# Optimization experiments

Hardware: AMD Instinct MI355X
Metric: run time of the kernel (lower is better)

Reference implementation:

```python
import jax, jax.numpy as jnp
import numpy as np

N = 4096      # nnode
F = 128       # feature_dim
E = 64        # embed_dim
P_EDGE = 0.01 # edge probability (~41 avg degree)
NEG = -9e15
ALPHA = 0.2   # leaky relu slope


def _xavier(key, shape):
    lim = float(np.sqrt(6.0 / (shape[0] + shape[1])))
    return jax.random.uniform(key, shape, minval=-lim, maxval=lim, dtype=jnp.float32)


def setup_inputs() -> dict:
    key = jax.random.key(0)
    ks = jax.random.split(key, 14)
    features = jax.random.normal(ks[0], (N, F), dtype=jnp.float32)
    eye = jnp.eye(N, dtype=jnp.float32)

    def make_adj(k):
        a = (jax.random.uniform(k, (N, N)) < P_EDGE).astype(jnp.float32)
        return jnp.maximum(a, eye)  # self loop so no empty rows

    return {
        "features": features,
        "geo_adj": make_adj(ks[1]),
        "forward_adj": make_adj(ks[2]),
        "backward_adj": make_adj(ks[3]),
        "weight": _xavier(ks[4], (E, F)),
        "Wf": _xavier(ks[5], (F, E)),
        "af1": jax.random.normal(ks[6], (E,), dtype=jnp.float32) * 0.1,
        "af2": jax.random.normal(ks[7], (E,), dtype=jnp.float32) * 0.1,
        "Wb": _xavier(ks[8], (F, E)),
        "ab1": jax.random.normal(ks[9], (E,), dtype=jnp.float32) * 0.1,
        "ab2": jax.random.normal(ks[10], (E,), dtype=jnp.float32) * 0.1,
        "Wg": _xavier(ks[11], (F, E)),
        "ag1": jax.random.normal(ks[12], (E,), dtype=jnp.float32) * 0.1,
        "ag2": jax.random.normal(ks[13], (E,), dtype=jnp.float32) * 0.1,
    }


def _mean_neighbors(adj, feat):
    # pre_weight: row-normalized neighbor averaging, (N,N) @ (N,F)
    deg = jnp.clip(jnp.sum(adj, axis=1, keepdims=True), 1.0, None)
    return (adj @ feat) / deg


def _attention(feat, mask_feat, adj, W, a1, a2):
    # GAT-style additive attention with masked softmax over neighbors
    h = feat @ W        # (N, E)
    hm = mask_feat @ W  # (N, E)
    e = jax.nn.leaky_relu((h @ a1)[:, None] + (hm @ a2)[None, :], negative_slope=ALPHA)  # (N, N)
    e = jnp.where(adj > 0, e, NEG)
    return jax.nn.softmax(e, axis=1)  # (N, N)


def reference(features, geo_adj, forward_adj, backward_adj, weight,
              Wf, af1, af2, Wb, ab1, ab2, Wg, ag1, ag2):
    t = features  # (N, F)
    mask_f = _mean_neighbors(forward_adj, t)
    mask_b = _mean_neighbors(backward_adj, t)
    mask_g = _mean_neighbors(geo_adj, t)

    w_f = _attention(t, mask_f, forward_adj, Wf, af1, af2)
    w_b = _attention(t, mask_b, backward_adj, Wb, ab1, ab2)
    w_g = _attention(t, mask_g, geo_adj, Wg, ag1, ag2)

    # get_mask_matrix_i/_j broadcast-mul + sum(1) == attn @ t (or attn.T @ t)
    x = weight @ t.T                  # (E, N)
    x_fwd = weight @ (w_f @ t).T      # mask_matrix_i
    x_bwd = weight @ (w_b.T @ t).T    # mask_matrix_j (transposed)
    x_geo = weight @ (w_g @ t).T      # mask_matrix_i

    return jnp.concatenate([x, x_fwd, x_bwd, x_geo], axis=0)  # (4E, N)
```

## Files before the change

### kernel.cpp

```cpp
#include <hip/hip_runtime.h>

#define NN 4096
#define FF 128
#define EE 64

typedef unsigned short u16;
typedef unsigned long long u64;
typedef float vf4 __attribute__((ext_vector_type(4)));

__device__ __forceinline__ float lrelu(float x) { return x > 0.f ? x : 0.2f * x; }

__global__ __launch_bounds__(256)
void k_feat(const float* __restrict__ t, const float* __restrict__ weight,
            const float* __restrict__ Wf, const float* __restrict__ af1, const float* __restrict__ af2,
            const float* __restrict__ Wb, const float* __restrict__ ab1, const float* __restrict__ ab2,
            const float* __restrict__ Wg, const float* __restrict__ ag1, const float* __restrict__ ag2,
            float* __restrict__ u, float* __restrict__ s1, float* __restrict__ p,
            float* __restrict__ out, int* __restrict__ ccnt)
{
    __shared__ float ww[64 * 129];
    __shared__ float tt[16 * 130];
    __shared__ float vv[6 * FF];
    __shared__ float uacc[64 * 17];
    const float* Ws[3]  = {Wf, Wb, Wg};
    const float* a1s[3] = {af1, ab1, ag1};
    const float* a2s[3] = {af2, ab2, ag2};
    int b = blockIdx.x, tid = threadIdx.x;
    int n0 = b * 16;
    if (b < 16) ccnt[b * 256 + tid] = 0;
    const float4* w4 = reinterpret_cast<const float4*>(weight);
    for (int i = tid; i < 2048; i += 256) {
        float4 v = w4[i];
        int fi = i * 4, e = fi >> 7, q = fi & 127;
        float* dst = &ww[e * 129 + q];
        dst[0] = v.x; dst[1] = v.y; dst[2] = v.z; dst[3] = v.w;
    }
    const float4* t4 = reinterpret_cast<const float4*>(t + (size_t)n0 * FF);
    for (int i = tid; i < 512; i += 256) {
        float4 v = t4[i];
        int fi = i * 4, nd = fi >> 7, q = fi & 127;
        float* dst = &tt[nd * 130 + q];
        dst[0] = v.x; dst[1] = v.y; dst[2] = v.z; dst[3] = v.w;
    }
    for (int idx = tid; idx < 6 * FF; idx += 256) {
        int vi = idx >> 7, f = idx & (FF - 1), dd = vi >> 1;
        const float* a = (vi & 1) ? a2s[dd] : a1s[dd];
        const float* W = Ws[dd] + (size_t)f * EE;
        float s = 0.f;
        #pragma unroll 8
        for (int e = 0; e < EE; ++e) s += W[e] * a[e];
        vv[idx] = s;
    }
    __syncthreads();
    int g = tid >> 6, lane = tid & 63;
    for (int k = 0; k < 4; ++k) {
        int nd = g * 4 + k;
        const float* trow = &tt[nd * 130];
        const float* wrow = &ww[lane * 129];
        float acc = 0.f;
        #pragma unroll 16
        for (int q = 0; q < 128; ++q) acc += wrow[q] * trow[q];
        u[(size_t)(n0 + nd) * EE + lane] = acc;
        uacc[lane * 17 + nd] = acc;
        float t0 = trow[lane], t1 = trow[64 + lane];
        for (int vi = 0; vi < 6; ++vi) {
            float x = t0 * vv[vi * FF + lane] + t1 * vv[vi * FF + 64 + lane];
            for (int off = 32; off; off >>= 1) x += __shfl_xor(x, off);
            if (lane == 0) {
                int dd = vi >> 1;
                if (vi & 1) p[dd * NN + n0 + nd] = x; else s1[dd * NN + n0 + nd] = x;
            }
        }
    }
    __syncthreads();
    int e = tid >> 2, io = (tid & 3) * 4;
    float* orow = out + (size_t)e * NN + n0 + io;
    orow[0] = uacc[e * 17 + io];
    orow[1] = uacc[e * 17 + io + 1];
    orow[2] = uacc[e * 17 + io + 2];
    orow[3] = uacc[e * 17 + io + 3];
}

__global__ __launch_bounds__(256, 8)
void k_scan(const float* __restrict__ Af, const float* __restrict__ Ab, const float* __restrict__ Ag,
            const float* __restrict__ p,
            u16* __restrict__ csr, int* __restrict__ cnt, float* __restrict__ s2,
            u16* __restrict__ csc, int* __restrict__ ccnt, int stride)
{
    int wid = threadIdx.x >> 6, lane = threadIdx.x & 63;
    int gr = blockIdx.x * 4 + wid;
    int d = gr >> 12, r = gr & (NN - 1);
    const float* A = d == 0 ? Af : (d == 1 ? Ab : Ag);
    const vf4* row4 = reinterpret_cast<const vf4*>(A + (size_t)r * NN);
    const float* pd = p + d * NN;

    u64 mask = 0ull;
    #pragma unroll
    for (int j = 0; j < 16; ++j) {
        vf4 L = __builtin_nontemporal_load(row4 + j * 64 + lane);
        unsigned mm = (L.x != 0.f ? 1u : 0u) | (L.y != 0.f ? 2u : 0u) |
                      (L.z != 0.f ? 4u : 0u) | (L.w != 0.f ? 8u : 0u);
        mask |= ((u64)mm) << (j * 4);
    }

    int lc = __popcll(mask);
    int sc = lc;
    for (int off = 1; off < 64; off <<= 1) {
        int o = __shfl_up(sc, off);
        if (lane >= off) sc += o;
    }
    int total = __shfl(sc, 63);
    int pos = sc - lc;
    u16* crow = csr + (size_t)gr * stride;
    float q = 0.f;
    u64 m = mask;
    while (m) {
        int b = __ffsll(m) - 1;
        m &= m - 1;
        int col = ((b >> 2) << 8) + (lane << 2) + (b & 3);
        if (pos < stride) crow[pos] = (u16)col;
        pos++;
        q += pd[col];
        if (d == 1) {
            int cp = atomicAdd(&ccnt[col], 1);
            if (cp < stride) csc[(size_t)col * stride + cp] = (u16)r;
        }
    }
    for (int off = 32; off; off >>= 1) q += __shfl_xor(q, off);
    if (lane == 0) {
        cnt[gr] = total;
        s2[gr] = q / fmaxf((float)total, 1.f);
    }
}

__global__ void k_zb(const float* __restrict__ s1, const float* __restrict__ s2,
                     const u16* __restrict__ csr, const int* __restrict__ cnt, int stride,
                     float* __restrict__ Zb)
{
    int tid = threadIdx.x, wave = tid >> 6, lane = tid & 63;
    int j = blockIdx.x * 4 + wave;
    int gr = NN + j;
    int nnz = min(cnt[gr], stride);
    const u16* crow = csr + (size_t)gr * stride;
    float s1j = s1[gr];
    const float* s2b = s2 + NN;
    float z = 0.f;
    if (lane < nnz)      z += __expf(lrelu(s1j + s2b[crow[lane]]));
    if (lane + 64 < nnz) z += __expf(lrelu(s1j + s2b[crow[lane + 64]]));
    for (int off = 32; off; off >>= 1) z += __shfl_xor(z, off);
    if (lane == 0) Zb[j] = z;
}

__global__ __launch_bounds__(256)
void k_out(const float* __restrict__ u,
           const float* __restrict__ s1, const float* __restrict__ s2,
           const float* __restrict__ Zb,
           const u16* __restrict__ csr, const int* __restrict__ cnt,
           const u16* __restrict__ csc, const int* __restrict__ ccnt, int stride,
           float* __restrict__ out)
{
    __shared__ float oacc[16 * 66];
    int gr0 = blockIdx.x * 16;
    int d = gr0 >> 12, i0 = gr0 & (NN - 1);
    int wid = threadIdx.x >> 6, lane = threadIdx.x & 63;
    for (int k = 0; k < 4; ++k) {
        int lr = k * 4 + wid;
        int i = i0 + lr;
        int gr = gr0 + lr;
        int nnz;
        int c0v = 0, c1v = 0;
        float w0v = 0.f, w1v = 0.f;
        if (d == 1) {
            nnz = min(ccnt[i], stride);
            const u16* cc = csc + (size_t)i * stride;
            float s2i = s2[NN + i];
            if (lane < nnz)      { int j = cc[lane];      c0v = j; w0v = __expf(lrelu(s1[NN + j] + s2i)) / Zb[j]; }
            if (lane + 64 < nnz) { int j = cc[lane + 64]; c1v = j; w1v = __expf(lrelu(s1[NN + j] + s2i)) / Zb[j]; }
        } else {
            nnz = min(cnt[gr], stride);
            const u16* crow = csr + (size_t)gr * stride;
            float s1i = s1[gr];
            const float* s2d = s2 + d * NN;
            float z = 0.f;
            if (lane < nnz)      { int c = crow[lane];      c0v = c; w0v = __expf(lrelu(s1i + s2d[c])); z += w0v; }
            if (lane + 64 < nnz) { int c = crow[lane + 64]; c1v = c; w1v = __expf(lrelu(s1i + s2d[c])); z += w1v; }
            for (int off = 32; off; off >>= 1) z += __shfl_xor(z, off);
            float invz = z > 0.f ? 1.f / z : 0.f;
            w0v *= invz; w1v *= invz;
        }
        float a0 = 0.f, a1 = 0.f;
        int n0 = nnz < 64 ? nnz : 64;
        int kk = 0;
        for (; kk + 1 < n0; kk += 2) {
            int ca = __shfl(c0v, kk), cb = __shfl(c0v, kk + 1);
            float wa = __shfl(w0v, kk), wb = __shfl(w0v, kk + 1);
            a0 += wa * u[(size_t)ca * EE + lane];
            a1 += wb * u[(size_t)cb * EE + lane];
        }
        if (kk < n0)
            a0 += __shfl(w0v, kk) * u[(size_t)__shfl(c0v, kk) * EE + lane];
        int n1 = nnz - 64;
        kk = 0;
        for (; kk + 1 < n1; kk += 2) {
            int ca = __shfl(c1v, kk), cb = __shfl(c1v, kk + 1);
            float wa = __shfl(w1v, kk), wb = __shfl(w1v, kk + 1);
            a0 += wa * u[(size_t)ca * EE + lane];
            a1 += wb * u[(size_t)cb * EE + lane];
        }
        if (kk < n1)
            a0 += __shfl(w1v, kk) * u[(size_t)__shfl(c1v, kk) * EE + lane];
        oacc[lr * 66 + lane] = a0 + a1;
    }
    __syncthreads();
    int e = threadIdx.x >> 2, io = (threadIdx.x & 3) * 4;
    int base = 64 + (d << 6);
    float* orow = out + (size_t)(base + e) * NN + i0 + io;
    orow[0] = oacc[(io    ) * 66 + e];
    orow[1] = oacc[(io + 1) * 66 + e];
    orow[2] = oacc[(io + 2) * 66 + e];
    orow[3] = oacc[(io + 3) * 66 + e];
}

extern "C" void kernel_launch(void* const* d_in, const int* in_sizes, int n_in,
                              void* d_out, int out_size, void* d_ws, size_t ws_size,
                              hipStream_t stream)
{
    const float* t   = (const float*)d_in[0];
    const float* Ag  = (const float*)d_in[1];
    const float* Af  = (const float*)d_in[2];
    const float* Ab  = (const float*)d_in[3];
    const float* W   = (const float*)d_in[4];
    const float* Wf  = (const float*)d_in[5];
    const float* af1 = (const float*)d_in[6];
    const float* af2 = (const float*)d_in[7];
    const float* Wb  = (const float*)d_in[8];
    const float* ab1 = (const float*)d_in[9];
    const float* ab2 = (const float*)d_in[10];
    const float* Wg  = (const float*)d_in[11];
    const float* ag1 = (const float*)d_in[12];
    const float* ag2 = (const float*)d_in[13];
    float* out = (float*)d_out;

    float* ws = (float*)d_ws;
    float* s1  = ws;
    float* p   = s1 + 3 * NN;
    float* s2  = p + 3 * NN;
    float* Zb  = s2 + 3 * NN;
    float* u   = Zb + NN;
    int*   cnt  = (int*)(u + (size_t)NN * EE);
    int*   ccnt = cnt + 3 * NN;
    u16*   csr  = (u16*)(ccnt + NN);

    size_t base_bytes = ((char*)csr) - ((char*)d_ws);
    int stride = 128;
    if (base_bytes + (size_t)4 * NN * 128 * 2 > ws_size) stride = 96;
    if (base_bytes + (size_t)4 * NN * 96 * 2 > ws_size)  stride = 64;
    u16* csc = csr + (size_t)3 * NN * stride;

    k_feat<<<NN / 16, 256, 0, stream>>>(t, W, Wf, af1, af2, Wb, ab1, ab2, Wg, ag1, ag2,
                                        u, s1, p, out, ccnt);
    k_scan<<<3 * NN / 4, 256, 0, stream>>>(Af, Ab, Ag, p, csr, cnt, s2, csc, ccnt, stride);
    k_zb<<<NN / 4, 256, 0, stream>>>(s1, s2, csr, cnt, stride, Zb);
    k_out<<<3 * NN / 16, 256, 0, stream>>>(u, s1, s2, Zb, csr, cnt, csc, ccnt, stride, out);
}
```

Measured before the change: 262.2 us.

## Parallelize attention-vector precompute per wave, pack s1/invZ, widen k_out blocks

In k_feat, the per-feature W·a dot products move from a serial 64-iteration loop per thread to one wave per item with a shuffle reduction, with the attention vectors staged in shared memory first. k_zb now writes a packed (s1, 1/Z) pair, so k_out does one float2 load and a multiply instead of two loads and a divide. k_out switches to 1024-thread blocks with one wave per row instead of four rows per wave, which exposes more parallelism, but the output store becomes scalar instead of four per thread.

```diff
diff --git a/kernel.cpp b/kernel.cpp
--- a/kernel.cpp
+++ b/kernel.cpp
@@ -21,13 +21,19 @@
     __shared__ float ww[64 * 129];
     __shared__ float tt[16 * 130];
     __shared__ float vv[6 * FF];
+    __shared__ float aa[6 * 64];
     __shared__ float uacc[64 * 17];
     const float* Ws[3]  = {Wf, Wb, Wg};
     const float* a1s[3] = {af1, ab1, ag1};
     const float* a2s[3] = {af2, ab2, ag2};
-    int b = blockIdx.x, tid = threadIdx.x;
+    int b = blockIdx.x, tid = threadIdx.x, wid = tid >> 6, lane = tid & 63;
     int n0 = b * 16;
     if (b < 16) ccnt[b * 256 + tid] = 0;
+    for (int i = tid; i < 384; i += 256) {
+        int vi = i >> 6, e = i & 63, dd = vi >> 1;
+        const float* a = (vi & 1) ? a2s[dd] : a1s[dd];
+        aa[i] = a[e];
+    }
     const float4* w4 = reinterpret_cast<const float4*>(weight);
     for (int i = tid; i < 2048; i += 256) {
         float4 v = w4[i];
@@ -42,19 +48,16 @@
         float* dst = &tt[nd * 130 + q];
         dst[0] = v.x; dst[1] = v.y; dst[2] = v.z; dst[3] = v.w;
     }
-    for (int idx = tid; idx < 6 * FF; idx += 256) {
-        int vi = idx >> 7, f = idx & (FF - 1), dd = vi >> 1;
-        const float* a = (vi & 1) ? a2s[dd] : a1s[dd];
-        const float* W = Ws[dd] + (size_t)f * EE;
-        float s = 0.f;
-        #pragma unroll 8
-        for (int e = 0; e < EE; ++e) s += W[e] * a[e];
-        vv[idx] = s;
-    }
-    __syncthreads();
-    int g = tid >> 6, lane = tid & 63;
+    __syncthreads();
+    for (int item = wid; item < 768; item += 4) {
+        int vi = item >> 7, f = item & 127, dd = vi >> 1;
+        float prod = Ws[dd][(size_t)f * EE + lane] * aa[vi * 64 + lane];
+        for (int off = 32; off; off >>= 1) prod += __shfl_xor(prod, off);
+        if (lane == 0) vv[vi * FF + f] = prod;
+    }
+    __syncthreads();
     for (int k = 0; k < 4; ++k) {
-        int nd = g * 4 + k;
+        int nd = wid * 4 + k;
         const float* trow = &tt[nd * 130];
         const float* wrow = &ww[lane * 129];
         float acc = 0.f;
@@ -135,7 +138,7 @@
 
 __global__ void k_zb(const float* __restrict__ s1, const float* __restrict__ s2,
                      const u16* __restrict__ csr, const int* __restrict__ cnt, int stride,
-                     float* __restrict__ Zb)
+                     float2* __restrict__ zpack)
 {
     int tid = threadIdx.x, wave = tid >> 6, lane = tid & 63;
     int j = blockIdx.x * 4 + wave;
@@ -148,13 +151,13 @@
     if (lane < nnz)      z += __expf(lrelu(s1j + s2b[crow[lane]]));
     if (lane + 64 < nnz) z += __expf(lrelu(s1j + s2b[crow[lane + 64]]));
     for (int off = 32; off; off >>= 1) z += __shfl_xor(z, off);
-    if (lane == 0) Zb[j] = z;
-}
-
-__global__ __launch_bounds__(256)
+    if (lane == 0) zpack[j] = make_float2(s1j, z > 0.f ? 1.f / z : 0.f);
+}
+
+__global__ __launch_bounds__(1024)
 void k_out(const float* __restrict__ u,
            const float* __restrict__ s1, const float* __restrict__ s2,
-           const float* __restrict__ Zb,
+           const float2* __restrict__ zpack,
            const u16* __restrict__ csr, const int* __restrict__ cnt,
            const u16* __restrict__ csc, const int* __restrict__ ccnt, int stride,
            float* __restrict__ out)
@@ -162,63 +165,57 @@
     __shared__ float oacc[16 * 66];
     int gr0 = blockIdx.x * 16;
     int d = gr0 >> 12, i0 = gr0 & (NN - 1);
-    int wid = threadIdx.x >> 6, lane = threadIdx.x & 63;
-    for (int k = 0; k < 4; ++k) {
-        int lr = k * 4 + wid;
-        int i = i0 + lr;
-        int gr = gr0 + lr;
-        int nnz;
-        int c0v = 0, c1v = 0;
-        float w0v = 0.f, w1v = 0.f;
-        if (d == 1) {
-            nnz = min(ccnt[i], stride);
-            const u16* cc = csc + (size_t)i * stride;
-            float s2i = s2[NN + i];
-            if (lane < nnz)      { int j = cc[lane];      c0v = j; w0v = __expf(lrelu(s1[NN + j] + s2i)) / Zb[j]; }
-            if (lane + 64 < nnz) { int j = cc[lane + 64]; c1v = j; w1v = __expf(lrelu(s1[NN + j] + s2i)) / Zb[j]; }
-        } else {
-            nnz = min(cnt[gr], stride);
-            const u16* crow = csr + (size_t)gr * stride;
-            float s1i = s1[gr];
-            const float* s2d = s2 + d * NN;
-            float z = 0.f;
-            if (lane < nnz)      { int c = crow[lane];      c0v = c; w0v = __expf(lrelu(s1i + s2d[c])); z += w0v; }
-            if (lane + 64 < nnz) { int c = crow[lane + 64]; c1v = c; w1v = __expf(lrelu(s1i + s2d[c])); z += w1v; }
-            for (int off = 32; off; off >>= 1) z += __shfl_xor(z, off);
-            float invz = z > 0.f ? 1.f / z : 0.f;
-            w0v *= invz; w1v *= invz;
-        }
-        float a0 = 0.f, a1 = 0.f;
-        int n0 = nnz < 64 ? nnz : 64;
-        int kk = 0;
-        for (; kk + 1 < n0; kk += 2) {
-            int ca = __shfl(c0v, kk), cb = __shfl(c0v, kk + 1);
-            float wa = __shfl(w0v, kk), wb = __shfl(w0v, kk + 1);
-            a0 += wa * u[(size_t)ca * EE + lane];
-            a1 += wb * u[(size_t)cb * EE + lane];
-        }
-        if (kk < n0)
-            a0 += __shfl(w0v, kk) * u[(size_t)__shfl(c0v, kk) * EE + lane];
-        int n1 = nnz - 64;
-        kk = 0;
-        for (; kk + 1 < n1; kk += 2) {
-            int ca = __shfl(c1v, kk), cb = __shfl(c1v, kk + 1);
-            float wa = __shfl(w1v, kk), wb = __shfl(w1v, kk + 1);
-            a0 += wa * u[(size_t)ca * EE + lane];
-            a1 += wb * u[(size_t)cb * EE + lane];
-        }
-        if (kk < n1)
-            a0 += __shfl(w1v, kk) * u[(size_t)__shfl(c1v, kk) * EE + lane];
-        oacc[lr * 66 + lane] = a0 + a1;
-    }
-    __syncthreads();
-    int e = threadIdx.x >> 2, io = (threadIdx.x & 3) * 4;
+    int tid = threadIdx.x, wid = tid >> 6, lane = tid & 63;
+    int lr = wid;
+    int i = i0 + lr;
+    int gr = gr0 + lr;
+    int nnz;
+    int c0v = 0, c1v = 0;
+    float w0v = 0.f, w1v = 0.f;
+    if (d == 1) {
+        nnz = min(ccnt[i], stride);
+        const u16* cc = csc + (size_t)i * stride;
+        float s2i = s2[NN + i];
+        if (lane < nnz)      { int j = cc[lane];      float2 z = zpack[j]; c0v = j; w0v = __expf(lrelu(z.x + s2i)) * z.y; }
+        if (lane + 64 < nnz) { int j = cc[lane + 64]; float2 z = zpack[j]; c1v = j; w1v = __expf(lrelu(z.x + s2i)) * z.y; }
+    } else {
+        nnz = min(cnt[gr], stride);
+        const u16* crow = csr + (size_t)gr * stride;
+        float s1i = s1[gr];
+        const float* s2d = s2 + d * NN;
+        float z = 0.f;
+        if (lane < nnz)      { int c = crow[lane];      c0v = c; w0v = __expf(lrelu(s1i + s2d[c])); z += w0v; }
+        if (lane + 64 < nnz) { int c = crow[lane + 64]; c1v = c; w1v = __expf(lrelu(s1i + s2d[c])); z += w1v; }
+        for (int off = 32; off; off >>= 1) z += __shfl_xor(z, off);
+        float invz = z > 0.f ? 1.f / z : 0.f;
+        w0v *= invz; w1v *= invz;
+    }
+    float a0 = 0.f, a1 = 0.f;
+    int n0 = nnz < 64 ? nnz : 64;
+    int kk = 0;
+    for (; kk + 1 < n0; kk += 2) {
+        int ca = __shfl(c0v, kk), cb = __shfl(c0v, kk + 1);
+        float wa = __shfl(w0v, kk), wb = __shfl(w0v, kk + 1);
+        a0 += wa * u[(size_t)ca * EE + lane];
+        a1 += wb * u[(size_t)cb * EE + lane];
+    }
+    if (kk < n0)
+        a0 += __shfl(w0v, kk) * u[(size_t)__shfl(c0v, kk) * EE + lane];
+    int n1 = nnz - 64;
+    kk = 0;
+    for (; kk + 1 < n1; kk += 2) {
+        int ca = __shfl(c1v, kk), cb = __shfl(c1v, kk + 1);
+        float wa = __shfl(w1v, kk), wb = __shfl(w1v, kk + 1);
+        a0 += wa * u[(size_t)ca * EE + lane];
+        a1 += wb * u[(size_t)cb * EE + lane];
+    }
+    if (kk < n1)
+        a0 += __shfl(w1v, kk) * u[(size_t)__shfl(c1v, kk) * EE + lane];
+    oacc[lr * 66 + lane] = a0 + a1;
+    __syncthreads();
+    int e = tid >> 4, io = tid & 15;
     int base = 64 + (d << 6);
-    float* orow = out + (size_t)(base + e) * NN + i0 + io;
-    orow[0] = oacc[(io    ) * 66 + e];
-    orow[1] = oacc[(io + 1) * 66 + e];
-    orow[2] = oacc[(io + 2) * 66 + e];
-    orow[3] = oacc[(io + 3) * 66 + e];
+    out[(size_t)(base + e) * NN + i0 + io] = oacc[io * 66 + e];
 }
 
 extern "C" void kernel_launch(void* const* d_in, const int* in_sizes, int n_in,
@@ -242,14 +239,14 @@
     float* out = (float*)d_out;
 
     float* ws = (float*)d_ws;
-    float* s1  = ws;
-    float* p   = s1 + 3 * NN;
-    float* s2  = p + 3 * NN;
-    float* Zb  = s2 + 3 * NN;
-    float* u   = Zb + NN;
-    int*   cnt  = (int*)(u + (size_t)NN * EE);
-    int*   ccnt = cnt + 3 * NN;
-    u16*   csr  = (u16*)(ccnt + NN);
+    float*  s1    = ws;
+    float*  p     = s1 + 3 * NN;
+    float*  s2    = p + 3 * NN;
+    float2* zpack = (float2*)(s2 + 3 * NN);
+    float*  u     = (float*)(zpack + NN);
+    int*    cnt   = (int*)(u + (size_t)NN * EE);
+    int*    ccnt  = cnt + 3 * NN;
+    u16*    csr   = (u16*)(ccnt + NN);
 
     size_t base_bytes = ((char*)csr) - ((char*)d_ws);
     int stride = 128;
@@ -260,6 +257,6 @@
     k_feat<<<NN / 16, 256, 0, stream>>>(t, W, Wf, af1, af2, Wb, ab1, ab2, Wg, ag1, ag2,
                                         u, s1, p, out, ccnt);
     k_scan<<<3 * NN / 4, 256, 0, stream>>>(Af, Ab, Ag, p, csr, cnt, s2, csc, ccnt, stride);
-    k_zb<<<NN / 4, 256, 0, stream>>>(s1, s2, csr, cnt, stride, Zb);
-    k_out<<<3 * NN / 16, 256, 0, stream>>>(u, s1, s2, Zb, csr, cnt, csc, ccnt, stride, out);
-}
+    k_zb<<<NN / 4, 256, 0, stream>>>(s1, s2, csr, cnt, stride, zpack);
+    k_out<<<3 * NN / 16, 1024, 0, stream>>>(u, s1, s2, zpack, csr, cnt, csc, ccnt, stride, out);
+}
```

Measured after the change: 329.6 us. 25.7% more time.
